# Kernel tuning notes

Hardware: AMD Instinct MI355X
Metric: run time of the kernel (lower is better)

Reference implementation:

```python
import jax, jax.numpy as jnp
import numpy as np

# Quantization constants (match init_kwargs)
A_SCALE = 0.05
W_SCALE = 0.01
A_QN = -127
A_QP = 127
B, IN_F, OUT_F = 32768, 1024, 1024


def setup_inputs() -> dict:
    key = jax.random.key(0)
    kx, kw, kb = jax.random.split(key, 3)
    x = jax.random.normal(kx, (B, IN_F), dtype=jnp.float32)
    # signed int4 weights in [-8, 7], packed two-per-byte: even cols -> low nibble, odd cols -> high nibble
    w_int4 = jax.random.randint(kw, (OUT_F, IN_F), -8, 8, dtype=jnp.int32)
    low = w_int4[:, 0::2] & 0xF
    high = w_int4[:, 1::2] & 0xF
    weight_packed = (low | (high << 4)).astype(jnp.uint8)  # [OUT_F, IN_F//2]
    bias = jax.random.normal(kb, (OUT_F,), dtype=jnp.float32)
    return {"x": x, "weight_packed": weight_packed, "bias": bias}


def _unpack_int4(packed):
    # packed: [OUT_F, IN_F//2] uint8 -> signed int4 weights [OUT_F, IN_F] as int8
    p = packed.astype(jnp.int32)
    low = p & 0xF
    high = (p >> 4) & 0xF
    low = low - jnp.where(low >= 8, 16, 0)
    high = high - jnp.where(high >= 8, 16, 0)
    w = jnp.stack([low, high], axis=-1).reshape(p.shape[0], -1)  # interleave -> [OUT_F, IN_F]
    return w.astype(jnp.int8)


def reference(x, weight_packed, bias):
    # Quantize activations to int8
    q = jnp.clip(jnp.round(x * (1.0 / A_SCALE)), A_QN, A_QP).astype(jnp.int8)  # [B, IN_F]
    w = _unpack_int4(weight_packed)  # [OUT_F, IN_F] int8 (values in [-8,7])
    acc = jax.lax.dot_general(
        q, w.T,
        dimension_numbers=(((1,), (0,)), ((), ())),
        preferred_element_type=jnp.int32,
    )  # [B, OUT_F] int32
    # Dequantize and add bias, output fp16
    out = acc.astype(jnp.float32) * (A_SCALE * W_SCALE) + bias[None, :]
    return out.astype(jnp.float16)
```

## Files before the change

### kernel.cpp

```cpp
#include <hip/hip_runtime.h>
#include <hip/hip_bf16.h>
#include <stdint.h>

#define M_DIM 32768
#define N_DIM 1024
#define K_DIM 1024

using int32x4 = __attribute__((ext_vector_type(4))) int;

__device__ __forceinline__ void gload_lds16(const void* g, void* l) {
  __builtin_amdgcn_global_load_lds(
      (const __attribute__((address_space(1))) void*)g,
      (__attribute__((address_space(3))) void*)l,
      16 , 0 , 0 );
}

__global__ __launch_bounds__(256) void quant_kernel(const float* __restrict__ x,
                                                    uint32_t* __restrict__ q) {
  const int g = blockIdx.x * 256 + threadIdx.x;
  const float4 v = ((const float4*)x)[g];
  int a0 = (int)rintf(fminf(fmaxf(v.x * 20.0f, -127.0f), 127.0f));
  int a1 = (int)rintf(fminf(fmaxf(v.y * 20.0f, -127.0f), 127.0f));
  int a2 = (int)rintf(fminf(fmaxf(v.z * 20.0f, -127.0f), 127.0f));
  int a3 = (int)rintf(fminf(fmaxf(v.w * 20.0f, -127.0f), 127.0f));
  q[g] = (uint32_t)(a0 & 0xFF) | ((uint32_t)(a1 & 0xFF) << 8) |
         ((uint32_t)(a2 & 0xFF) << 16) | ((uint32_t)(a3 & 0xFF) << 24);
}

__global__ __launch_bounds__(256) void unpack_kernel(const int4* __restrict__ wp,
                                                     uint2* __restrict__ w8) {
  const int g = blockIdx.x * 256 + threadIdx.x;
  const int4 p = wp[g];
  int w0 = ((p.x & 0xF) ^ 8) - 8;
  int w1 = (((p.x >> 4) & 0xF) ^ 8) - 8;
  int w2 = ((p.y & 0xF) ^ 8) - 8;
  int w3 = (((p.y >> 4) & 0xF) ^ 8) - 8;
  int w4 = ((p.z & 0xF) ^ 8) - 8;
  int w5 = (((p.z >> 4) & 0xF) ^ 8) - 8;
  int w6 = ((p.w & 0xF) ^ 8) - 8;
  int w7 = (((p.w >> 4) & 0xF) ^ 8) - 8;
  uint2 st;
  st.x = (uint32_t)(w0 & 0xFF) | ((uint32_t)(w1 & 0xFF) << 8) |
         ((uint32_t)(w2 & 0xFF) << 16) | ((uint32_t)(w3 & 0xFF) << 24);
  st.y = (uint32_t)(w4 & 0xFF) | ((uint32_t)(w5 & 0xFF) << 8) |
         ((uint32_t)(w6 & 0xFF) << 16) | ((uint32_t)(w7 & 0xFF) << 24);
  w8[g] = st;
}

__global__ __launch_bounds__(256) void gemm_kernel(const uint8_t* __restrict__ A,
                                                   const uint8_t* __restrict__ W,
                                                   const float* __restrict__ bias,
                                                   float* __restrict__ out) {
  __shared__ uint8_t sA[128 * 64];
  __shared__ uint8_t sB[128 * 64];

  const int tid = threadIdx.x;
  const int bx = blockIdx.x;
  const int n0 = (bx & 7) * 128;
  const int m0 = (bx >> 3) * 128;
  const int lane = tid & 63;
  const int wid = tid >> 6;
  const int wm = wid >> 1;
  const int wn = wid & 1;

  const int li0 = tid, li1 = 256 + tid;
  const int r0 = li0 >> 2, c0 = li0 & 3;
  const int r1 = li1 >> 2, c1 = li1 & 3;
  const int cg0 = c0 ^ ((r0 >> 1) & 3);
  const int cg1 = c1 ^ ((r1 >> 1) & 3);
  const uint8_t* gA0 = A + (size_t)(m0 + r0) * K_DIM + cg0 * 16;
  const uint8_t* gA1 = A + (size_t)(m0 + r1) * K_DIM + cg1 * 16;
  const uint8_t* gB0 = W + (size_t)(n0 + r0) * K_DIM + cg0 * 16;
  const uint8_t* gB1 = W + (size_t)(n0 + r1) * K_DIM + cg1 * 16;
  uint8_t* lA0 = sA + li0 * 16;
  uint8_t* lA1 = sA + li1 * 16;
  uint8_t* lB0 = sB + li0 * 16;
  uint8_t* lB1 = sB + li1 * 16;

  int32x4 acc[4][4] = {};

  const int q = lane >> 4;
  const int fr = lane & 15;

  for (int kk = 0; kk < K_DIM; kk += 64) {
    gload_lds16(gA0 + kk, lA0);
    gload_lds16(gA1 + kk, lA1);
    gload_lds16(gB0 + kk, lB0);
    gload_lds16(gB1 + kk, lB1);
    __syncthreads();

    int32x4 af[4], bf[4];
#pragma unroll
    for (int mt = 0; mt < 4; mt++) {
      const int r = wm * 64 + mt * 16 + fr;
      const int cc = q ^ ((r >> 1) & 3);
      af[mt] = *(const int32x4*)(sA + r * 64 + cc * 16);
    }
#pragma unroll
    for (int nt = 0; nt < 4; nt++) {
      const int r = wn * 64 + nt * 16 + fr;
      const int cc = q ^ ((r >> 1) & 3);
      bf[nt] = *(const int32x4*)(sB + r * 64 + cc * 16);
    }
#pragma unroll
    for (int mt = 0; mt < 4; mt++)
#pragma unroll
      for (int nt = 0; nt < 4; nt++)
        acc[mt][nt] = __builtin_amdgcn_mfma_i32_16x16x64_i8(af[mt], bf[nt], acc[mt][nt], 0, 0, 0);
    __syncthreads();
  }

  float bv[4];
#pragma unroll
  for (int nt = 0; nt < 4; nt++) bv[nt] = bias[n0 + wn * 64 + nt * 16 + fr];

  const int rowq = (lane >> 4) * 4;
#pragma unroll
  for (int mt = 0; mt < 4; mt++) {
#pragma unroll
    for (int nt = 0; nt < 4; nt++) {
      const int n_g = n0 + wn * 64 + nt * 16 + fr;
#pragma unroll
      for (int r = 0; r < 4; r++) {
        const int m_g = m0 + wm * 64 + mt * 16 + rowq + r;
        const float v = (float)acc[mt][nt][r] * 0.0005f + bv[nt];
        out[(size_t)m_g * N_DIM + n_g] = v;
      }
    }
  }
}

extern "C" void kernel_launch(void* const* d_in, const int* in_sizes, int n_in,
                              void* d_out, int out_size, void* d_ws, size_t ws_size,
                              hipStream_t stream) {
  const float* x = (const float*)d_in[0];
  const int4* wp = (const int4*)d_in[1];
  const float* bias = (const float*)d_in[2];
  float* out = (float*)d_out;

  uint8_t* A8 = (uint8_t*)d_ws;
  uint8_t* W8 = A8 + (size_t)M_DIM * K_DIM;

  quant_kernel<<<(M_DIM * K_DIM) / (4 * 256), 256, 0, stream>>>(x, (uint32_t*)A8);
  unpack_kernel<<<(N_DIM * K_DIM / 2) / (4 * 256), 256, 0, stream>>>(wp, (uint2*)W8);
  gemm_kernel<<<(M_DIM / 128) * (N_DIM / 128), 256, 0, stream>>>(A8, W8, bias, out);
}
```

Measured before the change: 277.0 us.

## Double-buffer GEMM LDS tiles, merge prep kernels, use nontemporal output stores

The GEMM main loop now uses two LDS buffers per operand. The next K-slice is issued with global_load_lds while the current slice feeds the MFMAs, which leaves one barrier per iteration instead of two. The activation quantize and weight unpack kernels are merged into a single launch with block-range dispatch, removing one launch. Output stores become nontemporal to reduce cache pollution. The cost is doubled LDS use per block, which may lower occupancy.

Measured after the change: 282.6 us. 2.0% more time.

```diff
diff --git a/kernel.cpp b/kernel.cpp
--- a/kernel.cpp
+++ b/kernel.cpp
@@ -15,44 +15,47 @@
       16 , 0 , 0 );
 }
 
-__global__ __launch_bounds__(256) void quant_kernel(const float* __restrict__ x,
-                                                    uint32_t* __restrict__ q) {
-  const int g = blockIdx.x * 256 + threadIdx.x;
-  const float4 v = ((const float4*)x)[g];
-  int a0 = (int)rintf(fminf(fmaxf(v.x * 20.0f, -127.0f), 127.0f));
-  int a1 = (int)rintf(fminf(fmaxf(v.y * 20.0f, -127.0f), 127.0f));
-  int a2 = (int)rintf(fminf(fmaxf(v.z * 20.0f, -127.0f), 127.0f));
-  int a3 = (int)rintf(fminf(fmaxf(v.w * 20.0f, -127.0f), 127.0f));
-  q[g] = (uint32_t)(a0 & 0xFF) | ((uint32_t)(a1 & 0xFF) << 8) |
-         ((uint32_t)(a2 & 0xFF) << 16) | ((uint32_t)(a3 & 0xFF) << 24);
-}
-
-__global__ __launch_bounds__(256) void unpack_kernel(const int4* __restrict__ wp,
-                                                     uint2* __restrict__ w8) {
-  const int g = blockIdx.x * 256 + threadIdx.x;
-  const int4 p = wp[g];
-  int w0 = ((p.x & 0xF) ^ 8) - 8;
-  int w1 = (((p.x >> 4) & 0xF) ^ 8) - 8;
-  int w2 = ((p.y & 0xF) ^ 8) - 8;
-  int w3 = (((p.y >> 4) & 0xF) ^ 8) - 8;
-  int w4 = ((p.z & 0xF) ^ 8) - 8;
-  int w5 = (((p.z >> 4) & 0xF) ^ 8) - 8;
-  int w6 = ((p.w & 0xF) ^ 8) - 8;
-  int w7 = (((p.w >> 4) & 0xF) ^ 8) - 8;
-  uint2 st;
-  st.x = (uint32_t)(w0 & 0xFF) | ((uint32_t)(w1 & 0xFF) << 8) |
-         ((uint32_t)(w2 & 0xFF) << 16) | ((uint32_t)(w3 & 0xFF) << 24);
-  st.y = (uint32_t)(w4 & 0xFF) | ((uint32_t)(w5 & 0xFF) << 8) |
-         ((uint32_t)(w6 & 0xFF) << 16) | ((uint32_t)(w7 & 0xFF) << 24);
-  w8[g] = st;
+__global__ __launch_bounds__(256) void prep_kernel(const float* __restrict__ x,
+                                                   const int4* __restrict__ wp,
+                                                   uint32_t* __restrict__ q,
+                                                   uint2* __restrict__ w8) {
+  const int bx = blockIdx.x;
+  const int tid = threadIdx.x;
+  if (bx < 512) {
+    const int g = bx * 256 + tid;
+    const int4 p = wp[g];
+    int w0 = ((p.x & 0xF) ^ 8) - 8;
+    int w1 = (((p.x >> 4) & 0xF) ^ 8) - 8;
+    int w2 = ((p.y & 0xF) ^ 8) - 8;
+    int w3 = (((p.y >> 4) & 0xF) ^ 8) - 8;
+    int w4 = ((p.z & 0xF) ^ 8) - 8;
+    int w5 = (((p.z >> 4) & 0xF) ^ 8) - 8;
+    int w6 = ((p.w & 0xF) ^ 8) - 8;
+    int w7 = (((p.w >> 4) & 0xF) ^ 8) - 8;
+    uint2 st;
+    st.x = (uint32_t)(w0 & 0xFF) | ((uint32_t)(w1 & 0xFF) << 8) |
+           ((uint32_t)(w2 & 0xFF) << 16) | ((uint32_t)(w3 & 0xFF) << 24);
+    st.y = (uint32_t)(w4 & 0xFF) | ((uint32_t)(w5 & 0xFF) << 8) |
+           ((uint32_t)(w6 & 0xFF) << 16) | ((uint32_t)(w7 & 0xFF) << 24);
+    w8[g] = st;
+  } else {
+    const int g = (bx - 512) * 256 + tid;
+    const float4 v = ((const float4*)x)[g];
+    int a0 = (int)rintf(fminf(fmaxf(v.x * 20.0f, -127.0f), 127.0f));
+    int a1 = (int)rintf(fminf(fmaxf(v.y * 20.0f, -127.0f), 127.0f));
+    int a2 = (int)rintf(fminf(fmaxf(v.z * 20.0f, -127.0f), 127.0f));
+    int a3 = (int)rintf(fminf(fmaxf(v.w * 20.0f, -127.0f), 127.0f));
+    q[g] = (uint32_t)(a0 & 0xFF) | ((uint32_t)(a1 & 0xFF) << 8) |
+           ((uint32_t)(a2 & 0xFF) << 16) | ((uint32_t)(a3 & 0xFF) << 24);
+  }
 }
 
 __global__ __launch_bounds__(256) void gemm_kernel(const uint8_t* __restrict__ A,
                                                    const uint8_t* __restrict__ W,
                                                    const float* __restrict__ bias,
                                                    float* __restrict__ out) {
-  __shared__ uint8_t sA[128 * 64];
-  __shared__ uint8_t sB[128 * 64];
+  __shared__ uint8_t sA[2][128 * 64];
+  __shared__ uint8_t sB[2][128 * 64];
 
   const int tid = threadIdx.x;
   const int bx = blockIdx.x;
@@ -72,42 +75,51 @@
   const uint8_t* gA1 = A + (size_t)(m0 + r1) * K_DIM + cg1 * 16;
   const uint8_t* gB0 = W + (size_t)(n0 + r0) * K_DIM + cg0 * 16;
   const uint8_t* gB1 = W + (size_t)(n0 + r1) * K_DIM + cg1 * 16;
-  uint8_t* lA0 = sA + li0 * 16;
-  uint8_t* lA1 = sA + li1 * 16;
-  uint8_t* lB0 = sB + li0 * 16;
-  uint8_t* lB1 = sB + li1 * 16;
+
+  gload_lds16(gA0, sA[0] + li0 * 16);
+  gload_lds16(gA1, sA[0] + li1 * 16);
+  gload_lds16(gB0, sB[0] + li0 * 16);
+  gload_lds16(gB1, sB[0] + li1 * 16);
 
   int32x4 acc[4][4] = {};
 
   const int q = lane >> 4;
   const int fr = lane & 15;
 
-  for (int kk = 0; kk < K_DIM; kk += 64) {
-    gload_lds16(gA0 + kk, lA0);
-    gload_lds16(gA1 + kk, lA1);
-    gload_lds16(gB0 + kk, lB0);
-    gload_lds16(gB1 + kk, lB1);
+#pragma unroll 1
+  for (int kk = 0; kk < 16; kk++) {
     __syncthreads();
+
+    if (kk < 15) {
+      const int off = (kk + 1) * 64;
+      const int nb = (kk + 1) & 1;
+      gload_lds16(gA0 + off, sA[nb] + li0 * 16);
+      gload_lds16(gA1 + off, sA[nb] + li1 * 16);
+      gload_lds16(gB0 + off, sB[nb] + li0 * 16);
+      gload_lds16(gB1 + off, sB[nb] + li1 * 16);
+    }
+
+    const uint8_t* pA = sA[kk & 1];
+    const uint8_t* pB = sB[kk & 1];
 
     int32x4 af[4], bf[4];
 #pragma unroll
     for (int mt = 0; mt < 4; mt++) {
       const int r = wm * 64 + mt * 16 + fr;
       const int cc = q ^ ((r >> 1) & 3);
-      af[mt] = *(const int32x4*)(sA + r * 64 + cc * 16);
+      af[mt] = *(const int32x4*)(pA + r * 64 + cc * 16);
     }
 #pragma unroll
     for (int nt = 0; nt < 4; nt++) {
       const int r = wn * 64 + nt * 16 + fr;
       const int cc = q ^ ((r >> 1) & 3);
-      bf[nt] = *(const int32x4*)(sB + r * 64 + cc * 16);
+      bf[nt] = *(const int32x4*)(pB + r * 64 + cc * 16);
     }
 #pragma unroll
     for (int mt = 0; mt < 4; mt++)
 #pragma unroll
       for (int nt = 0; nt < 4; nt++)
         acc[mt][nt] = __builtin_amdgcn_mfma_i32_16x16x64_i8(af[mt], bf[nt], acc[mt][nt], 0, 0, 0);
-    __syncthreads();
   }
 
   float bv[4];
@@ -124,7 +136,7 @@
       for (int r = 0; r < 4; r++) {
         const int m_g = m0 + wm * 64 + mt * 16 + rowq + r;
         const float v = (float)acc[mt][nt][r] * 0.0005f + bv[nt];
-        out[(size_t)m_g * N_DIM + n_g] = v;
+        __builtin_nontemporal_store(v, &out[(size_t)m_g * N_DIM + n_g]);
       }
     }
   }
@@ -141,7 +153,7 @@
   uint8_t* A8 = (uint8_t*)d_ws;
   uint8_t* W8 = A8 + (size_t)M_DIM * K_DIM;
 
-  quant_kernel<<<(M_DIM * K_DIM) / (4 * 256), 256, 0, stream>>>(x, (uint32_t*)A8);
-  unpack_kernel<<<(N_DIM * K_DIM / 2) / (4 * 256), 256, 0, stream>>>(wp, (uint2*)W8);
+  prep_kernel<<<512 + (M_DIM * K_DIM) / (4 * 256), 256, 0, stream>>>(
+      x, wp, (uint32_t*)A8, (uint2*)W8);
   gemm_kernel<<<(M_DIM / 128) * (N_DIM / 128), 256, 0, stream>>>(A8, W8, bias, out);
 }
```
